# Performance work log

Measured on AMD Instinct MI355X. Metric: run time of the kernel, lower is better.

## Reference

```python
import jax, jax.numpy as jnp
import numpy as np

N = 100_000      # nodes per type
E = 1_000_000    # edges per edge type
F_IN = 32        # raw feature dim
HID = 64         # hidden_channels
H, D = 2, 32     # num_heads, head_dim


def setup_inputs() -> dict:
    key = jax.random.key(0)
    ks = jax.random.split(key, 64)
    it = iter(range(64))
    def nrm(shape, scale=0.1):
        return jax.random.normal(ks[next(it)], shape, dtype=jnp.float32) * scale
    inp = {}
    inp['x_mac'] = jax.random.normal(ks[next(it)], (N, F_IN), dtype=jnp.float32)
    inp['x_buf'] = jax.random.normal(ks[next(it)], (N, F_IN), dtype=jnp.float32)
    inp['ei_m2b'] = jax.random.randint(ks[next(it)], (2, E), 0, N)
    inp['ei_b2m'] = jax.random.randint(ks[next(it)], (2, E), 0, N)
    for t in ('mac', 'buf'):
        inp[f'enc_w_{t}'] = nrm((F_IN, HID))
        inp[f'enc_b_{t}'] = jnp.zeros((HID,), jnp.float32)
        inp[f'enc_g_{t}'] = jnp.ones((HID,), jnp.float32)
        inp[f'enc_be_{t}'] = jnp.zeros((HID,), jnp.float32)
        for p in ('k', 'q', 'v'):
            inp[f'{p}_w_{t}'] = nrm((HID, HID))
            inp[f'{p}_b_{t}'] = jnp.zeros((HID,), jnp.float32)
        inp[f'o_w_{t}'] = nrm((HID, HID))
        inp[f'o_b_{t}'] = jnp.zeros((HID,), jnp.float32)
        inp[f'skip_{t}'] = jnp.ones((), jnp.float32)
    for r in ('m2b', 'b2m'):
        inp[f'a_{r}'] = nrm((H, D, D))
        inp[f'm_{r}'] = nrm((H, D, D))
        inp[f'p_{r}'] = jnp.ones((H,), jnp.float32)
    inp['ln_g'] = jnp.ones((HID,), jnp.float32)
    inp['ln_b'] = jnp.zeros((HID,), jnp.float32)
    return inp


def _ln(x, g, b, eps=1e-5):
    mu = jnp.mean(x, -1, keepdims=True)
    var = jnp.mean((x - mu) ** 2, -1, keepdims=True)
    return g * (x - mu) * jax.lax.rsqrt(var + eps) + b


def _seg_softmax(logits, seg, n):
    # logits: [E, H], seg: [E] dst ids. Numerically stable per-segment softmax.
    m = jax.ops.segment_max(logits, seg, num_segments=n)
    m = jnp.where(jnp.isfinite(m), m, 0.0)  # empty segments -> -inf
    e = jnp.exp(logits - m[seg])
    s = jax.ops.segment_sum(e, seg, num_segments=n)
    return e / (s[seg] + 1e-16)


def _hgt_edge(q_dst, k_src, v_src, a_rel, m_rel, p_rel, ei, n_dst):
    # q_dst:[Nd,H,D] k_src/v_src:[Ns,H,D] a_rel/m_rel:[H,D,D] p_rel:[H] ei:[2,E]
    src, dst = ei[0], ei[1]
    k = jnp.einsum('nhd,hde->nhe', k_src, a_rel)   # relation-transform keys
    v = jnp.einsum('nhd,hde->nhe', v_src, m_rel)   # relation-transform values
    alpha = (q_dst[dst] * k[src]).sum(-1) * p_rel / jnp.sqrt(jnp.float32(D))  # [E,H]
    alpha = _seg_softmax(alpha, dst, n_dst)
    msg = v[src] * alpha[..., None]                # [E,H,D]
    return jax.ops.segment_sum(msg, dst, num_segments=n_dst).reshape(n_dst, H * D)


def _forward(x_mac, x_buf, ei_m2b, ei_b2m,
             enc_w_mac, enc_b_mac, enc_g_mac, enc_be_mac,
             enc_w_buf, enc_b_buf, enc_g_buf, enc_be_buf,
             k_w_mac, k_b_mac, q_w_mac, q_b_mac, v_w_mac, v_b_mac,
             k_w_buf, k_b_buf, q_w_buf, q_b_buf, v_w_buf, v_b_buf,
             o_w_mac, o_b_mac, o_w_buf, o_b_buf, skip_mac, skip_buf,
             a_m2b, m_m2b, p_m2b, a_b2m, m_b2m, p_b2m, ln_g, ln_b):
    n_mac, n_buf = x_mac.shape[0], x_buf.shape[0]
    # per-type encoder: Linear -> LayerNorm -> ReLU (dropout = identity in eval)
    h_mac = jax.nn.relu(_ln(x_mac @ enc_w_mac + enc_b_mac, enc_g_mac, enc_be_mac))
    h_buf = jax.nn.relu(_ln(x_buf @ enc_w_buf + enc_b_buf, enc_g_buf, enc_be_buf))
    # HGTConv: per-type k/q/v projections -> [N,H,D]
    k_mac = (h_mac @ k_w_mac + k_b_mac).reshape(n_mac, H, D)
    q_mac = (h_mac @ q_w_mac + q_b_mac).reshape(n_mac, H, D)
    v_mac = (h_mac @ v_w_mac + v_b_mac).reshape(n_mac, H, D)
    k_buf = (h_buf @ k_w_buf + k_b_buf).reshape(n_buf, H, D)
    q_buf = (h_buf @ q_w_buf + q_b_buf).reshape(n_buf, H, D)
    v_buf = (h_buf @ v_w_buf + v_b_buf).reshape(n_buf, H, D)
    # per-edge-type attention + scatter-softmax + sum aggregate
    agg_buf = _hgt_edge(q_buf, k_mac, v_mac, a_m2b, m_m2b, p_m2b, ei_m2b, n_buf)
    agg_mac = _hgt_edge(q_mac, k_buf, v_buf, a_b2m, m_b2m, p_b2m, ei_b2m, n_mac)
    # per-dst-type output: out_lin(gelu(agg)), sigmoid-skip gating with input
    a_mac = jax.nn.gelu(agg_mac, approximate=False) @ o_w_mac + o_b_mac
    a_buf = jax.nn.gelu(agg_buf, approximate=False) @ o_w_buf + o_b_buf
    g_mac = jax.nn.sigmoid(skip_mac)
    g_buf = jax.nn.sigmoid(skip_buf)
    conv_mac = g_mac * a_mac + (1.0 - g_mac) * h_mac
    conv_buf = g_buf * a_buf + (1.0 - g_buf) * h_buf
    # module-level residual + shared LayerNorm
    y_mac = _ln(conv_mac + h_mac, ln_g, ln_b)
    y_buf = _ln(conv_buf + h_buf, ln_g, ln_b)
    return y_mac, y_buf


def reference(x_mac, x_buf, ei_m2b, ei_b2m,
              enc_w_mac, enc_b_mac, enc_g_mac, enc_be_mac,
              enc_w_buf, enc_b_buf, enc_g_buf, enc_be_buf,
              k_w_mac, k_b_mac, q_w_mac, q_b_mac, v_w_mac, v_b_mac,
              k_w_buf, k_b_buf, q_w_buf, q_b_buf, v_w_buf, v_b_buf,
              o_w_mac, o_b_mac, o_w_buf, o_b_buf, skip_mac, skip_buf,
              a_m2b, m_m2b, p_m2b, a_b2m, m_b2m, p_b2m, ln_g, ln_b):
    return _forward(x_mac, x_buf, ei_m2b, ei_b2m,
                    enc_w_mac, enc_b_mac, enc_g_mac, enc_be_mac,
                    enc_w_buf, enc_b_buf, enc_g_buf, enc_be_buf,
                    k_w_mac, k_b_mac, q_w_mac, q_b_mac, v_w_mac, v_b_mac,
                    k_w_buf, k_b_buf, q_w_buf, q_b_buf, v_w_buf, v_b_buf,
                    o_w_mac, o_b_mac, o_w_buf, o_b_buf, skip_mac, skip_buf,
                    a_m2b, m_m2b, p_m2b, a_b2m, m_b2m, p_b2m, ln_g, ln_b)
```

## Files before the change

kernel.cpp:

```cpp
#include <hip/hip_runtime.h>
#include <hip/hip_bf16.h>
#include <math.h>

#define NN 100000
#define NN2 200000
#define NE 1000000
#define FIN 32
#define HIDC 64

#define NB 782
#define NBP 1024
#define EPB 4096
#define SCGRID 489
#define CAP 3072
#define MAXIT 12
#define KQV_BLKS 1563

typedef unsigned int u32;
typedef unsigned short u16;

typedef __attribute__((ext_vector_type(8))) short bf16x8;
typedef __attribute__((ext_vector_type(4))) float f32x4;

__device__ __forceinline__ float wsum(float v) {
  #pragma unroll
  for (int off = 32; off; off >>= 1) v += __shfl_xor(v, off, 64);
  return v;
}

__device__ __forceinline__ u16 f2bf(float f) {
  union { float f; u32 u; } c; c.f = f;
  u32 u = c.u;
  return (u16)((u + 0x7FFFu + ((u >> 16) & 1u)) >> 16);
}

__device__ __forceinline__ float bf2f(u32 v) {
  union { u32 u; float f; } c; c.u = v << 16; return c.f;
}

__device__ __forceinline__ bf16x8 ldfrag(const u16* p) {
  uint4 v = *(const uint4*)p;
  union { uint4 u; bf16x8 b; } c; c.u = v; return c.b;
}

__device__ __forceinline__ void scan1024(u32* a, u32* wtot) {
  int t = threadIdx.x, lane = t & 63, wv = t >> 6;
  u32 v0 = a[t * 4 + 0], v1 = a[t * 4 + 1], v2 = a[t * 4 + 2], v3 = a[t * 4 + 3];
  u32 sum = v0 + v1 + v2 + v3;
  u32 x = sum;
  #pragma unroll
  for (int off = 1; off < 64; off <<= 1) {
    u32 y = __shfl_up(x, off, 64);
    if (lane >= off) x += y;
  }
  if (lane == 63) wtot[wv] = x;
  u32 excl = x - sum;
  __syncthreads();
  u32 wb = 0;
  #pragma unroll
  for (int w = 0; w < 4; w++) if (w < wv) wb += wtot[w];
  u32 b = wb + excl;
  a[t * 4 + 0] = b;
  a[t * 4 + 1] = b + v0;
  a[t * 4 + 2] = b + v0 + v1;
  a[t * 4 + 3] = b + v0 + v1 + v2;
}

__device__ __forceinline__ void edge_decode(
    int ee, const int* __restrict__ ei_m2b, const int* __restrict__ ei_b2m,
    int& src_g, int& dst_g) {
  if (ee < NE) {
    src_g = ei_m2b[ee];
    dst_g = NN + ei_m2b[NE + ee];
  } else {
    int e2 = ee - NE;
    src_g = NN + ei_b2m[e2];
    dst_g = ei_b2m[NE + e2];
  }
}

#define FUSE2_T (192 * 64 + 192)
__global__ __launch_bounds__(256) void k_fuse2(
    const float* __restrict__ qw0, const float* __restrict__ qb0,
    const float* __restrict__ kw0, const float* __restrict__ kb0,
    const float* __restrict__ vw0, const float* __restrict__ vb0,
    const float* __restrict__ ar0, const float* __restrict__ mr0,
    const float* __restrict__ p0,
    const float* __restrict__ qw1, const float* __restrict__ qb1,
    const float* __restrict__ kw1, const float* __restrict__ kb1,
    const float* __restrict__ vw1, const float* __restrict__ vb1,
    const float* __restrict__ ar1, const float* __restrict__ mr1,
    const float* __restrict__ p1,
    u16* __restrict__ WfTb, float* __restrict__ bfv) {
  int gidx = blockIdx.x * 256 + threadIdx.x;
  if (gidx >= 2 * FUSE2_T) return;
  int type = gidx >= FUSE2_T;
  int idx = gidx - type * FUSE2_T;
  const float* qw = type ? qw1 : qw0; const float* qb = type ? qb1 : qb0;
  const float* kw = type ? kw1 : kw0; const float* kb = type ? kb1 : kb0;
  const float* vw = type ? vw1 : vw0; const float* vb = type ? vb1 : vb0;
  const float* ar = type ? ar1 : ar0; const float* mr = type ? mr1 : mr0;
  const float* p  = type ? p1  : p0;
  if (idx < 192 * 64) {
    int c = idx >> 6, k = idx & 63;
    float o;
    if (c < 64) {
      o = qw[k * 64 + c];
    } else {
      int e = c & 63, hd = e >> 5, ee = e & 31;
      bool isK = c < 128;
      const float* M = isK ? ar : mr;
      const float* Wsrc = isK ? kw : vw;
      float s = 0.0f;
      #pragma unroll
      for (int d = 0; d < 32; ++d)
        s += Wsrc[k * 64 + hd * 32 + d] * M[hd * 32 * 32 + d * 32 + ee];
      if (isK) s *= p[hd] * 0.17677669529663687f;
      o = s;
    }
    WfTb[(size_t)type * 192 * 64 + c * 64 + k] = f2bf(o);
  } else {
    int c = idx - 192 * 64;
    float o;
    if (c < 64) {
      o = qb[c];
    } else {
      int e = c & 63, hd = e >> 5, ee = e & 31;
      bool isK = c < 128;
      const float* M = isK ? ar : mr;
      const float* Bb = isK ? kb : vb;
      float s = 0.0f;
      #pragma unroll
      for (int d = 0; d < 32; ++d)
        s += Bb[hd * 32 + d] * M[hd * 32 * 32 + d * 32 + ee];
      if (isK) s *= p[hd] * 0.17677669529663687f;
      o = s;
    }
    bfv[(size_t)type * 192 + c] = o;
  }
}

__global__ __launch_bounds__(256) void k_enc3(
    const float* __restrict__ x_mac, const float* __restrict__ x_buf,
    const float* __restrict__ w_mac, const float* __restrict__ b_mac,
    const float* __restrict__ g_mac, const float* __restrict__ be_mac,
    const float* __restrict__ w_buf, const float* __restrict__ b_buf,
    const float* __restrict__ g_buf, const float* __restrict__ be_buf,
    u16* __restrict__ hb) {
  __shared__ float xs[64][FIN + 1];
  __shared__ float ts[64][HIDC + 1];
  int t = threadIdx.x;
  int b = blockIdx.x;
  int type = b >= KQV_BLKS;
  int r0   = type ? (NN + (b - KQV_BLKS) * 64) : (b * 64);
  int rend = type ? NN2 : NN;
  const float* w  = type ? w_buf  : w_mac;
  const float* bb = type ? b_buf  : b_mac;
  const float* g  = type ? g_buf  : g_mac;
  const float* be = type ? be_buf : be_mac;
  const float* x  = type ? x_buf  : x_mac;
  int xoff = type ? NN : 0;
  for (int i = t; i < 64 * 8; i += 256) {
    int row = i >> 3, c4 = i & 7;
    int gr = r0 + row; if (gr >= rend) gr = rend - 1;
    float4 v = *(const float4*)&x[(size_t)(gr - xoff) * FIN + c4 * 4];
    xs[row][c4 * 4 + 0] = v.x; xs[row][c4 * 4 + 1] = v.y;
    xs[row][c4 * 4 + 2] = v.z; xs[row][c4 * 4 + 3] = v.w;
  }
  __syncthreads();
  int rg = t & 15, cg = t >> 4;
  float acc[4][4];
  #pragma unroll
  for (int c = 0; c < 4; c++) {
    float bv = bb[cg * 4 + c];
    #pragma unroll
    for (int r = 0; r < 4; r++) acc[r][c] = bv;
  }
  for (int k = 0; k < FIN; ++k) {
    float a0 = xs[rg * 4 + 0][k];
    float a1 = xs[rg * 4 + 1][k];
    float a2 = xs[rg * 4 + 2][k];
    float a3 = xs[rg * 4 + 3][k];
    float4 wv4 = *(const float4*)&w[k * HIDC + cg * 4];
    acc[0][0] = fmaf(a0, wv4.x, acc[0][0]); acc[0][1] = fmaf(a0, wv4.y, acc[0][1]);
    acc[0][2] = fmaf(a0, wv4.z, acc[0][2]); acc[0][3] = fmaf(a0, wv4.w, acc[0][3]);
    acc[1][0] = fmaf(a1, wv4.x, acc[1][0]); acc[1][1] = fmaf(a1, wv4.y, acc[1][1]);
    acc[1][2] = fmaf(a1, wv4.z, acc[1][2]); acc[1][3] = fmaf(a1, wv4.w, acc[1][3]);
    acc[2][0] = fmaf(a2, wv4.x, acc[2][0]); acc[2][1] = fmaf(a2, wv4.y, acc[2][1]);
    acc[2][2] = fmaf(a2, wv4.z, acc[2][2]); acc[2][3] = fmaf(a2, wv4.w, acc[2][3]);
    acc[3][0] = fmaf(a3, wv4.x, acc[3][0]); acc[3][1] = fmaf(a3, wv4.y, acc[3][1]);
    acc[3][2] = fmaf(a3, wv4.z, acc[3][2]); acc[3][3] = fmaf(a3, wv4.w, acc[3][3]);
  }
  #pragma unroll
  for (int r = 0; r < 4; r++)
    #pragma unroll
    for (int c = 0; c < 4; c++) ts[rg * 4 + r][cg * 4 + c] = acc[r][c];
  __syncthreads();
  int wv = t >> 6, ln = t & 63;
  for (int rr = wv; rr < 64; rr += 4) {
    int gr = r0 + rr;
    if (gr >= rend) break;
    float v = ts[rr][ln];
    float mu = wsum(v) * (1.0f / HIDC);
    float d = v - mu;
    float var = wsum(d * d) * (1.0f / HIDC);
    float yv = g[ln] * d * rsqrtf(var + 1e-5f) + be[ln];
    hb[(size_t)gr * HIDC + ln] = f2bf(fmaxf(yv, 0.0f));
  }
}

__global__ __launch_bounds__(256) void k_kqv4(
    const u16* __restrict__ hb, const u16* __restrict__ WfTb,
    const float* __restrict__ bfv,
    u16* __restrict__ qo, u32* __restrict__ kvt) {
  int t = threadIdx.x;
  int b = blockIdx.x;
  int type = b >= KQV_BLKS;
  int r0   = type ? (NN + (b - KQV_BLKS) * 64) : (b * 64);
  int rend = type ? NN2 : NN;
  const u16* WT = WfTb + (size_t)type * 192 * 64;
  const float* B = bfv + (size_t)type * 192;
  int w = t >> 6, l = t & 63;
  int lr = l & 15, lk = l >> 4;
  int arow = r0 + w * 16 + lr;
  int arowc = arow >= rend ? rend - 1 : arow;
  bf16x8 a0 = ldfrag(&hb[(size_t)arowc * 64 + lk * 8]);
  bf16x8 a1 = ldfrag(&hb[(size_t)arowc * 64 + 32 + lk * 8]);
  f32x4 acc[12];
  #pragma unroll
  for (int j = 0; j < 12; j++) {
    bf16x8 b0 = ldfrag(&WT[(size_t)(j * 16 + lr) * 64 + lk * 8]);
    bf16x8 b1 = ldfrag(&WT[(size_t)(j * 16 + lr) * 64 + 32 + lk * 8]);
    f32x4 c = {0.0f, 0.0f, 0.0f, 0.0f};
    c = __builtin_amdgcn_mfma_f32_16x16x32_bf16(a0, b0, c, 0, 0, 0);
    c = __builtin_amdgcn_mfma_f32_16x16x32_bf16(a1, b1, c, 0, 0, 0);
    acc[j] = c;
  }
  int orow0 = r0 + w * 16 + lk * 4;
  #pragma unroll
  for (int j = 0; j < 4; j++) {
    float bv = B[j * 16 + lr];
    #pragma unroll
    for (int r = 0; r < 4; r++) {
      int orow = orow0 + r;
      if (orow < rend)
        qo[(size_t)orow * 64 + j * 16 + lr] = f2bf(acc[j][r] + bv);
    }
  }
  #pragma unroll
  for (int j = 0; j < 4; j++) {
    float bk = B[64 + j * 16 + lr];
    float bv2 = B[128 + j * 16 + lr];
    #pragma unroll
    for (int r = 0; r < 4; r++) {
      int orow = orow0 + r;
      if (orow < rend) {
        u32 kv = (u32)f2bf(acc[4 + j][r] + bk) | ((u32)f2bf(acc[8 + j][r] + bv2) << 16);
        kvt[(size_t)orow * 64 + j * 16 + lr] = kv;
      }
    }
  }
}

__global__ __launch_bounds__(256) void k_out3(
    const u16* __restrict__ aggb, const u16* __restrict__ hb,
    const float* __restrict__ ow0, const float* __restrict__ ob0,
    const float* __restrict__ skip0,
    const float* __restrict__ ow1, const float* __restrict__ ob1,
    const float* __restrict__ skip1,
    const float* __restrict__ lg, const float* __restrict__ lb,
    float* __restrict__ y) {
  __shared__ float gs[64][65];
  int t = threadIdx.x;
  int b = blockIdx.x;
  int type = b >= KQV_BLKS;
  int r0   = type ? (NN + (b - KQV_BLKS) * 64) : (b * 64);
  int rend = type ? NN2 : NN;
  const float* ow = type ? ow1 : ow0;
  const float* ob = type ? ob1 : ob0;
  float gk = 1.0f / (1.0f + expf(-(type ? skip1 : skip0)[0]));
  for (int i = t; i < 64 * 8; i += 256) {
    int row = i >> 3, c8 = i & 7;
    int gr = r0 + row; if (gr >= rend) gr = rend - 1;
    uint4 v = *(const uint4*)&aggb[(size_t)gr * 64 + c8 * 8];
    u32 a[4] = { v.x, v.y, v.z, v.w };
    #pragma unroll
    for (int j = 0; j < 4; j++) {
      float f0 = bf2f(a[j] & 0xFFFFu);
      float f1 = bf2f(a[j] >> 16);
      gs[row][c8 * 8 + j * 2]     = 0.5f * f0 * (1.0f + erff(f0 * 0.70710678118654752f));
      gs[row][c8 * 8 + j * 2 + 1] = 0.5f * f1 * (1.0f + erff(f1 * 0.70710678118654752f));
    }
  }
  __syncthreads();
  int rg = t & 15, cg = t >> 4;
  float acc[4][4];
  #pragma unroll
  for (int c = 0; c < 4; c++) {
    float bv = ob[cg * 4 + c];
    #pragma unroll
    for (int r = 0; r < 4; r++) acc[r][c] = bv;
  }
  for (int k = 0; k < 64; ++k) {
    float a0 = gs[rg * 4 + 0][k];
    float a1 = gs[rg * 4 + 1][k];
    float a2 = gs[rg * 4 + 2][k];
    float a3 = gs[rg * 4 + 3][k];
    float4 wv4 = *(const float4*)&ow[k * 64 + cg * 4];
    acc[0][0] = fmaf(a0, wv4.x, acc[0][0]); acc[0][1] = fmaf(a0, wv4.y, acc[0][1]);
    acc[0][2] = fmaf(a0, wv4.z, acc[0][2]); acc[0][3] = fmaf(a0, wv4.w, acc[0][3]);
    acc[1][0] = fmaf(a1, wv4.x, acc[1][0]); acc[1][1] = fmaf(a1, wv4.y, acc[1][1]);
    acc[1][2] = fmaf(a1, wv4.z, acc[1][2]); acc[1][3] = fmaf(a1, wv4.w, acc[1][3]);
    acc[2][0] = fmaf(a2, wv4.x, acc[2][0]); acc[2][1] = fmaf(a2, wv4.y, acc[2][1]);
    acc[2][2] = fmaf(a2, wv4.z, acc[2][2]); acc[2][3] = fmaf(a2, wv4.w, acc[2][3]);
    acc[3][0] = fmaf(a3, wv4.x, acc[3][0]); acc[3][1] = fmaf(a3, wv4.y, acc[3][1]);
    acc[3][2] = fmaf(a3, wv4.z, acc[3][2]); acc[3][3] = fmaf(a3, wv4.w, acc[3][3]);
  }
  float tv[4][4];
  float c2 = 2.0f - gk;
  #pragma unroll
  for (int r = 0; r < 4; r++) {
    int gr = r0 + rg * 4 + r; if (gr >= rend) gr = rend - 1;
    uint2 hv = *(const uint2*)&hb[(size_t)gr * 64 + cg * 4];
    float h0 = bf2f(hv.x & 0xFFFFu), h1 = bf2f(hv.x >> 16);
    float h2 = bf2f(hv.y & 0xFFFFu), h3 = bf2f(hv.y >> 16);
    tv[r][0] = fmaf(gk, acc[r][0], c2 * h0);
    tv[r][1] = fmaf(gk, acc[r][1], c2 * h1);
    tv[r][2] = fmaf(gk, acc[r][2], c2 * h2);
    tv[r][3] = fmaf(gk, acc[r][3], c2 * h3);
  }
  __syncthreads();
  #pragma unroll
  for (int r = 0; r < 4; r++)
    #pragma unroll
    for (int c = 0; c < 4; c++) gs[rg * 4 + r][cg * 4 + c] = tv[r][c];
  __syncthreads();
  int wv = t >> 6, ln = t & 63;
  for (int rr = wv; rr < 64; rr += 4) {
    int gr = r0 + rr;
    if (gr >= rend) break;
    float v = gs[rr][ln];
    float mu = wsum(v) * (1.0f / HIDC);
    float d = v - mu;
    float var = wsum(d * d) * (1.0f / HIDC);
    y[(size_t)gr * HIDC + ln] = lg[ln] * d * rsqrtf(var + 1e-5f) + lb[ln];
  }
}

__global__ __launch_bounds__(256) void k_bscatter2(
    const int* __restrict__ ei_m2b, const int* __restrict__ ei_b2m,
    u32* __restrict__ gcursor, u32* __restrict__ bpairs) {
  __shared__ u32 hist[NBP];
  __shared__ u32 loff[NBP];
  __shared__ u32 gbase[NBP];
  __shared__ u32 wtot[4];
  __shared__ u32 pairs[EPB];
  __shared__ u16 sbuck[EPB];
  int tid = threadIdx.x;
  for (int i = tid; i < NBP; i += 256) hist[i] = 0;
  __syncthreads();
  int base_e = blockIdx.x * EPB;
  u32 pk[EPB / 256];
  u16 bk[EPB / 256];
  u16 rk[EPB / 256];
  #pragma unroll
  for (int i = 0; i < EPB / 256; i++) {
    int ee = base_e + i * 256 + tid;
    if (ee < 2 * NE) {
      int src_g, dst_g;
      edge_decode(ee, ei_m2b, ei_b2m, src_g, dst_g);
      u32 b = (u32)dst_g >> 8;
      pk[i] = ((u32)(dst_g & 255) << 18) | (u32)src_g;
      bk[i] = (u16)b;
      rk[i] = (u16)atomicAdd(&hist[b], 1u);
    } else {
      bk[i] = 0xFFFFu;
    }
  }
  __syncthreads();
  for (int i = tid; i < NBP; i += 256) loff[i] = hist[i];
  __syncthreads();
  scan1024(loff, wtot);
  __syncthreads();
  #pragma unroll
  for (int i = 0; i < EPB / 256; i++) {
    if (bk[i] != 0xFFFFu) {
      u32 s = loff[bk[i]] + rk[i];
      pairs[s] = pk[i];
      sbuck[s] = bk[i];
    }
  }
  __syncthreads();
  for (int b = tid; b < NBP; b += 256) {
    u32 c = hist[b];
    gbase[b] = c ? atomicAdd(&gcursor[b], c) : 0u;
  }
  __syncthreads();
  int nval = 2 * NE - base_e;
  if (nval > EPB) nval = EPB;
  for (int s = tid; s < nval; s += 256) {
    u32 b = sbuck[s];
    u32 slot = gbase[b] + (s - loff[b]);
    if (slot < CAP) bpairs[(size_t)b * CAP + slot] = pairs[s];
  }
}

__global__ __launch_bounds__(256) void k_bedge3(
    const u32* __restrict__ gcursor, const u32* __restrict__ bpairs,
    const u16* __restrict__ q, const u32* __restrict__ kvt,
    u16* __restrict__ aggb) {
  __shared__ u32 srt[CAP];
  __shared__ u32 hist[64];
  __shared__ u32 rowptr[65];
  int tid = threadIdx.x;
  int b = blockIdx.x >> 2;
  u32 qr = blockIdx.x & 3;
  u32 cnt = gcursor[b];
  int n = (int)(cnt > CAP ? CAP : cnt);
  if (tid < 64) hist[tid] = 0;
  __syncthreads();
  u32 pk[MAXIT];
  #pragma unroll
  for (int it = 0; it < MAXIT; it++) {
    pk[it] = 0xFFFFFFFFu;
    int i = tid + it * 256;
    if (i < n) {
      u32 p = bpairs[(size_t)b * CAP + i];
      u32 ld = p >> 18;
      if ((ld >> 6) == qr) {
        atomicAdd(&hist[ld & 63], 1u);
        pk[it] = p;
      }
    }
  }
  __syncthreads();
  if (tid < 64) {
    u32 v = hist[tid];
    u32 x = v;
    #pragma unroll
    for (int off = 1; off < 64; off <<= 1) {
      u32 y = __shfl_up(x, off, 64);
      if (tid >= off) x += y;
    }
    rowptr[tid] = x - v;
    if (tid == 63) rowptr[64] = x;
  }
  __syncthreads();
  if (tid < 64) hist[tid] = rowptr[tid];
  __syncthreads();
  #pragma unroll
  for (int it = 0; it < MAXIT; it++) {
    u32 p = pk[it];
    if (p != 0xFFFFFFFFu) {
      u32 pos = atomicAdd(&hist[(p >> 18) & 63], 1u);
      srt[pos] = p & 0x3FFFFu;
    }
  }
  __syncthreads();
  int grp = tid >> 4, t = tid & 15;
  for (int ld = grp; ld < 64; ld += 16) {
    int dst_g = (b << 8) + ((int)qr << 6) + ld;
    if (dst_g >= NN2) continue;
    u32 j0 = rowptr[ld], j1 = rowptr[ld + 1];
    uint2 qp = *(const uint2*)&q[(size_t)dst_g * 64 + t * 4];
    float q0 = bf2f(qp.x & 0xFFFFu), q1 = bf2f(qp.x >> 16);
    float q2 = bf2f(qp.y & 0xFFFFu), q3 = bf2f(qp.y >> 16);
    float m = -1e30f, s = 0.0f;
    float a0 = 0.0f, a1 = 0.0f, a2 = 0.0f, a3 = 0.0f;
    u32 j = j0;
    for (; j + 2 <= j1; j += 2) {
      u32 s0 = srt[j], s1 = srt[j + 1];
      uint4 w0 = *(const uint4*)&kvt[(size_t)s0 * 64 + t * 4];
      uint4 w1 = *(const uint4*)&kvt[(size_t)s1 * 64 + t * 4];
      {
        float k0 = bf2f(w0.x & 0xFFFFu), v0 = bf2f(w0.x >> 16);
        float k1 = bf2f(w0.y & 0xFFFFu), v1 = bf2f(w0.y >> 16);
        float k2 = bf2f(w0.z & 0xFFFFu), v2 = bf2f(w0.z >> 16);
        float k3 = bf2f(w0.w & 0xFFFFu), v3 = bf2f(w0.w >> 16);
        float prod = fmaf(q3, k3, fmaf(q2, k2, fmaf(q1, k1, q0 * k0)));
        prod += __shfl_xor(prod, 1, 64);
        prod += __shfl_xor(prod, 2, 64);
        prod += __shfl_xor(prod, 4, 64);
        float mn = fmaxf(m, prod);
        float c = __expf(m - mn);
        float we = __expf(prod - mn);
        s = fmaf(s, c, we);
        a0 = fmaf(a0, c, we * v0);
        a1 = fmaf(a1, c, we * v1);
        a2 = fmaf(a2, c, we * v2);
        a3 = fmaf(a3, c, we * v3);
        m = mn;
      }
      {
        float k0 = bf2f(w1.x & 0xFFFFu), v0 = bf2f(w1.x >> 16);
        float k1 = bf2f(w1.y & 0xFFFFu), v1 = bf2f(w1.y >> 16);
        float k2 = bf2f(w1.z & 0xFFFFu), v2 = bf2f(w1.z >> 16);
        float k3 = bf2f(w1.w & 0xFFFFu), v3 = bf2f(w1.w >> 16);
        float prod = fmaf(q3, k3, fmaf(q2, k2, fmaf(q1, k1, q0 * k0)));
        prod += __shfl_xor(prod, 1, 64);
        prod += __shfl_xor(prod, 2, 64);
        prod += __shfl_xor(prod, 4, 64);
        float mn = fmaxf(m, prod);
        float c = __expf(m - mn);
        float we = __expf(prod - mn);
        s = fmaf(s, c, we);
        a0 = fmaf(a0, c, we * v0);
        a1 = fmaf(a1, c, we * v1);
        a2 = fmaf(a2, c, we * v2);
        a3 = fmaf(a3, c, we * v3);
        m = mn;
      }
    }
    if (j < j1) {
      u32 s0 = srt[j];
      uint4 w0 = *(const uint4*)&kvt[(size_t)s0 * 64 + t * 4];
      float k0 = bf2f(w0.x & 0xFFFFu), v0 = bf2f(w0.x >> 16);
      float k1 = bf2f(w0.y & 0xFFFFu), v1 = bf2f(w0.y >> 16);
      float k2 = bf2f(w0.z & 0xFFFFu), v2 = bf2f(w0.z >> 16);
      float k3 = bf2f(w0.w & 0xFFFFu), v3 = bf2f(w0.w >> 16);
      float prod = fmaf(q3, k3, fmaf(q2, k2, fmaf(q1, k1, q0 * k0)));
      prod += __shfl_xor(prod, 1, 64);
      prod += __shfl_xor(prod, 2, 64);
      prod += __shfl_xor(prod, 4, 64);
      float mn = fmaxf(m, prod);
      float c = __expf(m - mn);
      float we = __expf(prod - mn);
      s = fmaf(s, c, we);
      a0 = fmaf(a0, c, we * v0);
      a1 = fmaf(a1, c, we * v1);
      a2 = fmaf(a2, c, we * v2);
      a3 = fmaf(a3, c, we * v3);
      m = mn;
    }
    float inv = 1.0f / (s + 1e-16f);
    u32 o0 = (u32)f2bf(a0 * inv) | ((u32)f2bf(a1 * inv) << 16);
    u32 o1 = (u32)f2bf(a2 * inv) | ((u32)f2bf(a3 * inv) << 16);
    uint2 o = { o0, o1 };
    *(uint2*)&aggb[(size_t)dst_g * 64 + t * 4] = o;
  }
}

extern "C" void kernel_launch(void* const* d_in, const int* in_sizes, int n_in,
                              void* d_out, int out_size, void* d_ws, size_t ws_size,
                              hipStream_t stream) {
  const float* x_mac     = (const float*)d_in[0];
  const float* x_buf     = (const float*)d_in[1];
  const int*   ei_m2b    = (const int*)d_in[2];
  const int*   ei_b2m    = (const int*)d_in[3];
  const float* enc_w_mac = (const float*)d_in[4];
  const float* enc_b_mac = (const float*)d_in[5];
  const float* enc_g_mac = (const float*)d_in[6];
  const float* enc_be_mac= (const float*)d_in[7];
  const float* k_w_mac   = (const float*)d_in[8];
  const float* k_b_mac   = (const float*)d_in[9];
  const float* q_w_mac   = (const float*)d_in[10];
  const float* q_b_mac   = (const float*)d_in[11];
  const float* v_w_mac   = (const float*)d_in[12];
  const float* v_b_mac   = (const float*)d_in[13];
  const float* o_w_mac   = (const float*)d_in[14];
  const float* o_b_mac   = (const float*)d_in[15];
  const float* skip_mac  = (const float*)d_in[16];
  const float* enc_w_buf = (const float*)d_in[17];
  const float* enc_b_buf = (const float*)d_in[18];
  const float* enc_g_buf = (const float*)d_in[19];
  const float* enc_be_buf= (const float*)d_in[20];
  const float* k_w_buf   = (const float*)d_in[21];
  const float* k_b_buf   = (const float*)d_in[22];
  const float* q_w_buf   = (const float*)d_in[23];
  const float* q_b_buf   = (const float*)d_in[24];
  const float* v_w_buf   = (const float*)d_in[25];
  const float* v_b_buf   = (const float*)d_in[26];
  const float* o_w_buf   = (const float*)d_in[27];
  const float* o_b_buf   = (const float*)d_in[28];
  const float* skip_buf  = (const float*)d_in[29];
  const float* a_m2b     = (const float*)d_in[30];
  const float* m_m2b     = (const float*)d_in[31];
  const float* p_m2b     = (const float*)d_in[32];
  const float* a_b2m     = (const float*)d_in[33];
  const float* m_b2m     = (const float*)d_in[34];
  const float* p_b2m     = (const float*)d_in[35];
  const float* ln_g      = (const float*)d_in[36];
  const float* ln_b      = (const float*)d_in[37];

  char* ws = (char*)d_ws;
  size_t off = 0;
  auto take = [&](size_t bytes) -> char* {
    char* p = ws + off;
    off = (off + bytes + 255) & ~(size_t)255;
    return p;
  };
  u16*   hb      = (u16*)take((size_t)NN2 * HIDC * 2);
  u16*   aggb    = (u16*)take((size_t)NN2 * HIDC * 2);
  u16*   q       = (u16*)take((size_t)NN2 * HIDC * 2);
  u32*   kvt     = (u32*)take((size_t)NN2 * HIDC * 4);
  u16*   WfTb    = (u16*)take((size_t)2 * 192 * 64 * 2);
  float* bfv     = (float*)take((size_t)2 * 192 * 4);
  u32*   gcursor = (u32*)take((size_t)NBP * 4);
  u32*   bpairs  = (u32*)take((size_t)NB * CAP * 4);

  const int tile_grid  = 2 * KQV_BLKS;
  const int fuse2_grid = (2 * FUSE2_T + 255) / 256;

  k_fuse2<<<fuse2_grid, 256, 0, stream>>>(
      q_w_mac, q_b_mac, k_w_mac, k_b_mac, v_w_mac, v_b_mac, a_m2b, m_m2b, p_m2b,
      q_w_buf, q_b_buf, k_w_buf, k_b_buf, v_w_buf, v_b_buf, a_b2m, m_b2m, p_b2m,
      WfTb, bfv);
  hipMemsetAsync(gcursor, 0, (size_t)NBP * 4, stream);
  k_bscatter2<<<SCGRID, 256, 0, stream>>>(ei_m2b, ei_b2m, gcursor, bpairs);
  k_enc3<<<tile_grid, 256, 0, stream>>>(
      x_mac, x_buf,
      enc_w_mac, enc_b_mac, enc_g_mac, enc_be_mac,
      enc_w_buf, enc_b_buf, enc_g_buf, enc_be_buf, hb);
  k_kqv4<<<tile_grid, 256, 0, stream>>>(hb, WfTb, bfv, q, kvt);
  k_bedge3<<<4 * NB, 256, 0, stream>>>(gcursor, bpairs, q, kvt, aggb);
  k_out3<<<tile_grid, 256, 0, stream>>>(
      aggb, hb, o_w_mac, o_b_mac, skip_mac, o_w_buf, o_b_buf, skip_buf,
      ln_g, ln_b, (float*)d_out);
}
```

Before: 279.1 us.

## Split bucket scatter per relation, fold cursor reset into fuse kernel, unroll edge loop

The bucket scatter now runs one block per 2048 edges of a single relation. Each block only touches that relation's 391-bucket destination range, so the shared histogram, scan and atomics shrink to 512 entries and the per-edge relation branch goes away. The gcursor memset is folded into k_fuse2, which removes one launch. The edge aggregation loop is unrolled by four so that more kvt gathers are in flight, which costs extra registers.

```diff
diff --git a/kernel.cpp b/kernel.cpp
--- a/kernel.cpp
+++ b/kernel.cpp
@@ -10,8 +10,8 @@
 
 #define NB 782
 #define NBP 1024
-#define EPB 4096
-#define SCGRID 489
+#define EPB2 2048
+#define SC2 489
 #define CAP 3072
 #define MAXIT 12
 #define KQV_BLKS 1563
@@ -41,42 +41,6 @@
 __device__ __forceinline__ bf16x8 ldfrag(const u16* p) {
   uint4 v = *(const uint4*)p;
   union { uint4 u; bf16x8 b; } c; c.u = v; return c.b;
-}
-
-__device__ __forceinline__ void scan1024(u32* a, u32* wtot) {
-  int t = threadIdx.x, lane = t & 63, wv = t >> 6;
-  u32 v0 = a[t * 4 + 0], v1 = a[t * 4 + 1], v2 = a[t * 4 + 2], v3 = a[t * 4 + 3];
-  u32 sum = v0 + v1 + v2 + v3;
-  u32 x = sum;
-  #pragma unroll
-  for (int off = 1; off < 64; off <<= 1) {
-    u32 y = __shfl_up(x, off, 64);
-    if (lane >= off) x += y;
-  }
-  if (lane == 63) wtot[wv] = x;
-  u32 excl = x - sum;
-  __syncthreads();
-  u32 wb = 0;
-  #pragma unroll
-  for (int w = 0; w < 4; w++) if (w < wv) wb += wtot[w];
-  u32 b = wb + excl;
-  a[t * 4 + 0] = b;
-  a[t * 4 + 1] = b + v0;
-  a[t * 4 + 2] = b + v0 + v1;
-  a[t * 4 + 3] = b + v0 + v1 + v2;
-}
-
-__device__ __forceinline__ void edge_decode(
-    int ee, const int* __restrict__ ei_m2b, const int* __restrict__ ei_b2m,
-    int& src_g, int& dst_g) {
-  if (ee < NE) {
-    src_g = ei_m2b[ee];
-    dst_g = NN + ei_m2b[NE + ee];
-  } else {
-    int e2 = ee - NE;
-    src_g = NN + ei_b2m[e2];
-    dst_g = ei_b2m[NE + e2];
-  }
 }
 
 #define FUSE2_T (192 * 64 + 192)
@@ -91,8 +55,10 @@
     const float* __restrict__ vw1, const float* __restrict__ vb1,
     const float* __restrict__ ar1, const float* __restrict__ mr1,
     const float* __restrict__ p1,
-    u16* __restrict__ WfTb, float* __restrict__ bfv) {
+    u16* __restrict__ WfTb, float* __restrict__ bfv,
+    u32* __restrict__ gcursor) {
   int gidx = blockIdx.x * 256 + threadIdx.x;
+  if (gidx < NBP) gcursor[gidx] = 0;
   if (gidx >= 2 * FUSE2_T) return;
   int type = gidx >= FUSE2_T;
   int idx = gidx - type * FUSE2_T;
@@ -347,43 +313,65 @@
   }
 }
 
-__global__ __launch_bounds__(256) void k_bscatter2(
+__global__ __launch_bounds__(256) void k_bscatter3(
     const int* __restrict__ ei_m2b, const int* __restrict__ ei_b2m,
     u32* __restrict__ gcursor, u32* __restrict__ bpairs) {
-  __shared__ u32 hist[NBP];
-  __shared__ u32 loff[NBP];
-  __shared__ u32 gbase[NBP];
+  __shared__ u32 hist[512];
+  __shared__ u32 loff[512];
+  __shared__ u32 gbase[512];
   __shared__ u32 wtot[4];
-  __shared__ u32 pairs[EPB];
-  __shared__ u16 sbuck[EPB];
+  __shared__ u32 pairs[EPB2];
+  __shared__ u16 sbuck[EPB2];
   int tid = threadIdx.x;
-  for (int i = tid; i < NBP; i += 256) hist[i] = 0;
-  __syncthreads();
-  int base_e = blockIdx.x * EPB;
-  u32 pk[EPB / 256];
-  u16 bk[EPB / 256];
-  u16 rk[EPB / 256];
-  #pragma unroll
-  for (int i = 0; i < EPB / 256; i++) {
+  int blk = blockIdx.x;
+  int rel = blk >= SC2;
+  const int* ei = rel ? ei_b2m : ei_m2b;
+  int srcadd = rel ? NN : 0;
+  int dstadd = rel ? 0 : NN;
+  u32 base   = rel ? 0u : 390u;
+  int base_e = (rel ? blk - SC2 : blk) * EPB2;
+  for (int i = tid; i < 512; i += 256) hist[i] = 0;
+  __syncthreads();
+  u32 pk[EPB2 / 256];
+  u16 bk[EPB2 / 256];
+  u16 rk[EPB2 / 256];
+  #pragma unroll
+  for (int i = 0; i < EPB2 / 256; i++) {
     int ee = base_e + i * 256 + tid;
-    if (ee < 2 * NE) {
-      int src_g, dst_g;
-      edge_decode(ee, ei_m2b, ei_b2m, src_g, dst_g);
-      u32 b = (u32)dst_g >> 8;
-      pk[i] = ((u32)(dst_g & 255) << 18) | (u32)src_g;
-      bk[i] = (u16)b;
-      rk[i] = (u16)atomicAdd(&hist[b], 1u);
+    if (ee < NE) {
+      int s = ei[ee] + srcadd;
+      int d = ei[NE + ee] + dstadd;
+      u32 lb = ((u32)d >> 8) - base;
+      pk[i] = ((u32)(d & 255) << 18) | (u32)s;
+      bk[i] = (u16)lb;
+      rk[i] = (u16)atomicAdd(&hist[lb], 1u);
     } else {
       bk[i] = 0xFFFFu;
     }
   }
   __syncthreads();
-  for (int i = tid; i < NBP; i += 256) loff[i] = hist[i];
-  __syncthreads();
-  scan1024(loff, wtot);
-  __syncthreads();
-  #pragma unroll
-  for (int i = 0; i < EPB / 256; i++) {
+  {
+    int lane = tid & 63, wv = tid >> 6;
+    u32 v0 = hist[tid * 2], v1 = hist[tid * 2 + 1];
+    u32 sum = v0 + v1;
+    u32 x = sum;
+    #pragma unroll
+    for (int off = 1; off < 64; off <<= 1) {
+      u32 yv = __shfl_up(x, off, 64);
+      if (lane >= off) x += yv;
+    }
+    if (lane == 63) wtot[wv] = x;
+    u32 excl = x - sum;
+    __syncthreads();
+    u32 wb = 0;
+    #pragma unroll
+    for (int w = 0; w < 4; w++) if (w < wv) wb += wtot[w];
+    loff[tid * 2]     = wb + excl;
+    loff[tid * 2 + 1] = wb + excl + v0;
+  }
+  __syncthreads();
+  #pragma unroll
+  for (int i = 0; i < EPB2 / 256; i++) {
     if (bk[i] != 0xFFFFu) {
       u32 s = loff[bk[i]] + rk[i];
       pairs[s] = pk[i];
@@ -391,19 +379,39 @@
     }
   }
   __syncthreads();
-  for (int b = tid; b < NBP; b += 256) {
-    u32 c = hist[b];
-    gbase[b] = c ? atomicAdd(&gcursor[b], c) : 0u;
-  }
-  __syncthreads();
-  int nval = 2 * NE - base_e;
-  if (nval > EPB) nval = EPB;
+  for (int lb = tid; lb < 512; lb += 256) {
+    u32 c = hist[lb];
+    gbase[lb] = c ? atomicAdd(&gcursor[base + lb], c) : 0u;
+  }
+  __syncthreads();
+  int nval = NE - base_e;
+  if (nval > EPB2) nval = EPB2;
   for (int s = tid; s < nval; s += 256) {
-    u32 b = sbuck[s];
-    u32 slot = gbase[b] + (s - loff[b]);
-    if (slot < CAP) bpairs[(size_t)b * CAP + slot] = pairs[s];
-  }
-}
+    u32 lb = sbuck[s];
+    u32 slot = gbase[lb] + (s - loff[lb]);
+    if (slot < CAP) bpairs[(size_t)(base + lb) * CAP + slot] = pairs[s];
+  }
+}
+
+#define EDGE_STEP(W) {                                                        \
+    float k0 = bf2f(W.x & 0xFFFFu), v0 = bf2f(W.x >> 16);                     \
+    float k1 = bf2f(W.y & 0xFFFFu), v1 = bf2f(W.y >> 16);                     \
+    float k2 = bf2f(W.z & 0xFFFFu), v2 = bf2f(W.z >> 16);                     \
+    float k3 = bf2f(W.w & 0xFFFFu), v3 = bf2f(W.w >> 16);                     \
+    float prod = fmaf(q3, k3, fmaf(q2, k2, fmaf(q1, k1, q0 * k0)));           \
+    prod += __shfl_xor(prod, 1, 64);                                          \
+    prod += __shfl_xor(prod, 2, 64);                                          \
+    prod += __shfl_xor(prod, 4, 64);                                          \
+    float mn = fmaxf(m, prod);                                                \
+    float c = __expf(m - mn);                                                 \
+    float we = __expf(prod - mn);                                             \
+    s = fmaf(s, c, we);                                                       \
+    a0 = fmaf(a0, c, we * v0);                                                \
+    a1 = fmaf(a1, c, we * v1);                                                \
+    a2 = fmaf(a2, c, we * v2);                                                \
+    a3 = fmaf(a3, c, we * v3);                                                \
+    m = mn;                                                                   \
+  }
 
 __global__ __launch_bounds__(256) void k_bedge3(
     const u32* __restrict__ gcursor, const u32* __restrict__ bpairs,
@@ -468,69 +476,24 @@
     float m = -1e30f, s = 0.0f;
     float a0 = 0.0f, a1 = 0.0f, a2 = 0.0f, a3 = 0.0f;
     u32 j = j0;
+    for (; j + 4 <= j1; j += 4) {
+      u32 s0 = srt[j], s1 = srt[j + 1], s2 = srt[j + 2], s3 = srt[j + 3];
+      uint4 w0 = *(const uint4*)&kvt[(size_t)s0 * 64 + t * 4];
+      uint4 w1 = *(const uint4*)&kvt[(size_t)s1 * 64 + t * 4];
+      uint4 w2 = *(const uint4*)&kvt[(size_t)s2 * 64 + t * 4];
+      uint4 w3 = *(const uint4*)&kvt[(size_t)s3 * 64 + t * 4];
+      EDGE_STEP(w0); EDGE_STEP(w1); EDGE_STEP(w2); EDGE_STEP(w3);
+    }
     for (; j + 2 <= j1; j += 2) {
       u32 s0 = srt[j], s1 = srt[j + 1];
       uint4 w0 = *(const uint4*)&kvt[(size_t)s0 * 64 + t * 4];
       uint4 w1 = *(const uint4*)&kvt[(size_t)s1 * 64 + t * 4];
-      {
-        float k0 = bf2f(w0.x & 0xFFFFu), v0 = bf2f(w0.x >> 16);
-        float k1 = bf2f(w0.y & 0xFFFFu), v1 = bf2f(w0.y >> 16);
-        float k2 = bf2f(w0.z & 0xFFFFu), v2 = bf2f(w0.z >> 16);
-        float k3 = bf2f(w0.w & 0xFFFFu), v3 = bf2f(w0.w >> 16);
-        float prod = fmaf(q3, k3, fmaf(q2, k2, fmaf(q1, k1, q0 * k0)));
-        prod += __shfl_xor(prod, 1, 64);
-        prod += __shfl_xor(prod, 2, 64);
-        prod += __shfl_xor(prod, 4, 64);
-        float mn = fmaxf(m, prod);
-        float c = __expf(m - mn);
-        float we = __expf(prod - mn);
-        s = fmaf(s, c, we);
-        a0 = fmaf(a0, c, we * v0);
-        a1 = fmaf(a1, c, we * v1);
-        a2 = fmaf(a2, c, we * v2);
-        a3 = fmaf(a3, c, we * v3);
-        m = mn;
-      }
-      {
-        float k0 = bf2f(w1.x & 0xFFFFu), v0 = bf2f(w1.x >> 16);
-        float k1 = bf2f(w1.y & 0xFFFFu), v1 = bf2f(w1.y >> 16);
-        float k2 = bf2f(w1.z & 0xFFFFu), v2 = bf2f(w1.z >> 16);
-        float k3 = bf2f(w1.w & 0xFFFFu), v3 = bf2f(w1.w >> 16);
-        float prod = fmaf(q3, k3, fmaf(q2, k2, fmaf(q1, k1, q0 * k0)));
-        prod += __shfl_xor(prod, 1, 64);
-        prod += __shfl_xor(prod, 2, 64);
-        prod += __shfl_xor(prod, 4, 64);
-        float mn = fmaxf(m, prod);
-        float c = __expf(m - mn);
-        float we = __expf(prod - mn);
-        s = fmaf(s, c, we);
-        a0 = fmaf(a0, c, we * v0);
-        a1 = fmaf(a1, c, we * v1);
-        a2 = fmaf(a2, c, we * v2);
-        a3 = fmaf(a3, c, we * v3);
-        m = mn;
-      }
+      EDGE_STEP(w0); EDGE_STEP(w1);
     }
     if (j < j1) {
       u32 s0 = srt[j];
       uint4 w0 = *(const uint4*)&kvt[(size_t)s0 * 64 + t * 4];
-      float k0 = bf2f(w0.x & 0xFFFFu), v0 = bf2f(w0.x >> 16);
-      float k1 = bf2f(w0.y & 0xFFFFu), v1 = bf2f(w0.y >> 16);
-      float k2 = bf2f(w0.z & 0xFFFFu), v2 = bf2f(w0.z >> 16);
-      float k3 = bf2f(w0.w & 0xFFFFu), v3 = bf2f(w0.w >> 16);
-      float prod = fmaf(q3, k3, fmaf(q2, k2, fmaf(q1, k1, q0 * k0)));
-      prod += __shfl_xor(prod, 1, 64);
-      prod += __shfl_xor(prod, 2, 64);
-      prod += __shfl_xor(prod, 4, 64);
-      float mn = fmaxf(m, prod);
-      float c = __expf(m - mn);
-      float we = __expf(prod - mn);
-      s = fmaf(s, c, we);
-      a0 = fmaf(a0, c, we * v0);
-      a1 = fmaf(a1, c, we * v1);
-      a2 = fmaf(a2, c, we * v2);
-      a3 = fmaf(a3, c, we * v3);
-      m = mn;
+      EDGE_STEP(w0);
     }
     float inv = 1.0f / (s + 1e-16f);
     u32 o0 = (u32)f2bf(a0 * inv) | ((u32)f2bf(a1 * inv) << 16);
@@ -604,9 +567,8 @@
   k_fuse2<<<fuse2_grid, 256, 0, stream>>>(
       q_w_mac, q_b_mac, k_w_mac, k_b_mac, v_w_mac, v_b_mac, a_m2b, m_m2b, p_m2b,
       q_w_buf, q_b_buf, k_w_buf, k_b_buf, v_w_buf, v_b_buf, a_b2m, m_b2m, p_b2m,
-      WfTb, bfv);
-  hipMemsetAsync(gcursor, 0, (size_t)NBP * 4, stream);
-  k_bscatter2<<<SCGRID, 256, 0, stream>>>(ei_m2b, ei_b2m, gcursor, bpairs);
+      WfTb, bfv, gcursor);
+  k_bscatter3<<<2 * SC2, 256, 0, stream>>>(ei_m2b, ei_b2m, gcursor, bpairs);
   k_enc3<<<tile_grid, 256, 0, stream>>>(
       x_mac, x_buf,
       enc_w_mac, enc_b_mac, enc_g_mac, enc_be_mac,
```

Measured after the change: 287.6 us. +3.0%, slower.
